# Kernel optimization log

Hardware: AMD Instinct MI355X
Metric: run time of the kernel (lower is better)

## Reference

```python
import jax, jax.numpy as jnp
import numpy as np

B, S, E, H = 8, 1024, 1024, 16
D = E // H          # head_dim = 64
FF = 4 * E          # mlp hidden = 4096
EPS = 1e-5


def setup_inputs() -> dict:
    key = jax.random.key(0)
    ks = jax.random.split(key, 12)
    s_e = 1.0 / np.sqrt(E)
    s_ff = 1.0 / np.sqrt(FF)
    return {
        "x": jax.random.normal(ks[0], (B, S, E), jnp.float32),
        # per-head q/k/v projections stacked: [H, E, D] (math layout: y = x @ W + b)
        "Wq": jax.random.normal(ks[1], (H, E, D), jnp.float32) * s_e,
        "bq": jnp.zeros((H, D), jnp.float32),
        "Wk": jax.random.normal(ks[2], (H, E, D), jnp.float32) * s_e,
        "bk": jnp.zeros((H, D), jnp.float32),
        "Wv": jax.random.normal(ks[3], (H, E, D), jnp.float32) * s_e,
        "bv": jnp.zeros((H, D), jnp.float32),
        # output projection [E, E]
        "Wo": jax.random.normal(ks[4], (E, E), jnp.float32) * s_e,
        "bo": jnp.zeros((E,), jnp.float32),
        # layernorms
        "g1": jnp.ones((E,), jnp.float32),
        "beta1": jnp.zeros((E,), jnp.float32),
        "g2": jnp.ones((E,), jnp.float32),
        "beta2": jnp.zeros((E,), jnp.float32),
        # MLP
        "W1": jax.random.normal(ks[5], (E, FF), jnp.float32) * s_e,
        "c1": jnp.zeros((FF,), jnp.float32),
        "W2": jax.random.normal(ks[6], (FF, E), jnp.float32) * s_ff,
        "c2": jnp.zeros((E,), jnp.float32),
    }


def _layernorm(x, g, b):
    mu = jnp.mean(x, axis=-1, keepdims=True)
    var = jnp.mean(jnp.square(x - mu), axis=-1, keepdims=True)
    return (x - mu) * jax.lax.rsqrt(var + EPS) * g + b


def _block(x, Wq, bq, Wk, bk, Wv, bv, Wo, bo, g1, beta1, g2, beta2, W1, c1, W2, c2):
    # --- attention sublayer (pre-norm) ---
    xn = _layernorm(x, g1, beta1)
    # all heads at once (equivalent to the per-head Python loop)
    q = jnp.einsum("bse,hed->bhsd", xn, Wq) + bq[:, None, :]
    k = jnp.einsum("bse,hed->bhsd", xn, Wk) + bk[:, None, :]
    v = jnp.einsum("bse,hed->bhsd", xn, Wv) + bv[:, None, :]
    scale = D ** -0.5
    scores = jnp.einsum("bhsd,bhtd->bhst", q, k) * scale  # [B,H,S,S]
    w = jax.nn.softmax(scores, axis=-1)
    ctx = jnp.einsum("bhst,bhtd->bhsd", w, v)             # [B,H,S,D]
    ctx = ctx.transpose(0, 2, 1, 3).reshape(x.shape[0], x.shape[1], E)  # concat heads
    attn_out = ctx @ Wo + bo
    x = x + attn_out
    # --- MLP sublayer (pre-norm) ---
    xn = _layernorm(x, g2, beta2)
    h = jax.nn.gelu(xn @ W1 + c1, approximate=False)
    return x + (h @ W2 + c2)


def reference(x, Wq, bq, Wk, bk, Wv, bv, Wo, bo, g1, beta1, g2, beta2, W1, c1, W2, c2):
    return _block(x, Wq, bq, Wk, bk, Wv, bv, Wo, bo, g1, beta1, g2, beta2, W1, c1, W2, c2)
```

## Files before the change

### kernel.cpp

```cpp
#include <hip/hip_runtime.h>
#include <math.h>


typedef _Float16 h16;
typedef __attribute__((ext_vector_type(8))) _Float16 f16x8;
typedef __attribute__((ext_vector_type(4))) float f32x4;

__device__ __forceinline__ void gl2lds16(const void* g, void* l) {
  __builtin_amdgcn_global_load_lds(
      (const __attribute__((address_space(1))) void*)g,
      (__attribute__((address_space(3))) void*)l, 16, 0, 0);
}

__global__ __launch_bounds__(256) void repack_kernel(
    const float* __restrict__ Wq, const float* __restrict__ Wk,
    const float* __restrict__ Wv, const float* __restrict__ Wo,
    const float* __restrict__ W1, const float* __restrict__ W2,
    const float* __restrict__ bq, const float* __restrict__ bk,
    const float* __restrict__ bv,
    h16* __restrict__ WqkvT, h16* __restrict__ WoT, h16* __restrict__ W1T,
    h16* __restrict__ W2T, float* __restrict__ bqkv)
{
  const int t = blockIdx.x;
  const int tid = threadIdx.x;
  if (t == 3072) {
    for (int i = tid; i < 3072; i += 256)
      bqkv[i] = (i < 1024) ? bq[i] : (i < 2048 ? bk[i - 1024] : bv[i - 2048]);
    return;
  }
  __shared__ float ld[64 * 65];

  const float* src; h16* dst;
  int sRS, dRS, k0, sn0, dn0;
  if (t < 768) {
    const int m = t >> 8, tt = t & 255, h = tt >> 4, tk = tt & 15;
    src = ((m == 0) ? Wq : (m == 1) ? Wk : Wv) + (size_t)h * 65536;
    dst = WqkvT; sRS = 64; dRS = 1024;
    k0 = tk * 64; sn0 = 0; dn0 = m * 1024 + h * 64;
  } else if (t < 1024) {
    const int tt = t - 768, tk = tt >> 4, tn = tt & 15;
    src = Wo; dst = WoT; sRS = 1024; dRS = 1024;
    k0 = tk * 64; sn0 = tn * 64; dn0 = tn * 64;
  } else if (t < 2048) {
    const int tt = t - 1024, tk = tt >> 6, tn = tt & 63;
    src = W1; dst = W1T; sRS = 4096; dRS = 1024;
    k0 = tk * 64; sn0 = tn * 64; dn0 = tn * 64;
  } else {
    const int tt = t - 2048, tk = tt >> 4, tn = tt & 15;
    src = W2; dst = W2T; sRS = 1024; dRS = 4096;
    k0 = tk * 64; sn0 = tn * 64; dn0 = tn * 64;
  }

  #pragma unroll
  for (int p = 0; p < 16; ++p) {
    const int idx = p * 256 + tid;
    const int r = idx >> 6, c = idx & 63;
    ld[c * 65 + r] = src[(size_t)(k0 + r) * sRS + sn0 + c];
  }
  __syncthreads();
  #pragma unroll
  for (int p = 0; p < 8; ++p) {
    const int idx = p * 512 + tid * 2;
    const int n = idx >> 6, k = idx & 63;
    union { unsigned int u; h16 e[2]; } pk;
    pk.e[0] = (h16)ld[n * 65 + k];
    pk.e[1] = (h16)ld[n * 65 + k + 1];
    *(unsigned int*)&dst[(size_t)(dn0 + n) * dRS + k0 + k] = pk.u;
  }
}

template <int IT>
__global__ __launch_bounds__(256) void ln_kernel(
    const void* __restrict__ in, const float* __restrict__ gw,
    const float* __restrict__ bw, h16* __restrict__ outp)
{
  const int row = blockIdx.x;
  const int tid = threadIdx.x;
  float v[4];
  if (IT == 0) {
    const float* p = (const float*)in + (size_t)row * 1024 + tid * 4;
    float4 tt = *(const float4*)p;
    v[0] = tt.x; v[1] = tt.y; v[2] = tt.z; v[3] = tt.w;
  } else {
    const h16* p = (const h16*)in + (size_t)row * 1024 + tid * 4;
    union { uint2 u; h16 h[4]; } raw;
    raw.u = *(const uint2*)p;
    v[0] = (float)raw.h[0]; v[1] = (float)raw.h[1];
    v[2] = (float)raw.h[2]; v[3] = (float)raw.h[3];
  }
  float s = v[0] + v[1] + v[2] + v[3];
  float ss = v[0]*v[0] + v[1]*v[1] + v[2]*v[2] + v[3]*v[3];
  #pragma unroll
  for (int off = 32; off >= 1; off >>= 1) {
    s += __shfl_down(s, off);
    ss += __shfl_down(ss, off);
  }
  __shared__ float red[8];
  const int w = tid >> 6;
  if ((tid & 63) == 0) { red[w] = s; red[4 + w] = ss; }
  __syncthreads();
  s = red[0] + red[1] + red[2] + red[3];
  ss = red[4] + red[5] + red[6] + red[7];
  const float mean = s * (1.0f / 1024.0f);
  const float var = ss * (1.0f / 1024.0f) - mean * mean;
  const float inv = rsqrtf(fmaxf(var, 0.0f) + 1e-5f);
  union { uint2 u; h16 h[4]; } pk;
  #pragma unroll
  for (int i = 0; i < 4; ++i)
    pk.h[i] = (h16)((v[i] - mean) * inv * gw[tid * 4 + i] + bw[tid * 4 + i]);
  *(uint2*)(outp + (size_t)row * 1024 + tid * 4) = pk.u;
}

template <int MODE>
__global__ __launch_bounds__(256) void gemm_bt(
    const h16* __restrict__ A, const h16* __restrict__ BT,
    const float* __restrict__ bias, const void* __restrict__ res,
    void* __restrict__ out, int M, int N, int K)
{
  __shared__ __align__(16) h16 As[128 * 32];
  __shared__ __align__(16) h16 Bs[128 * 32];
  const int tid = threadIdx.x;
  const int m0 = blockIdx.y * 128, n0 = blockIdx.x * 128;
  const int lane = tid & 63, w = tid >> 6;
  const int l15 = lane & 15, quad = lane >> 4;
  const int wm = (w >> 1) * 64, wn = (w & 1) * 64;

  f32x4 zero = {0.f, 0.f, 0.f, 0.f};
  f32x4 acc[4][4];
  #pragma unroll
  for (int a = 0; a < 4; ++a)
    #pragma unroll
    for (int b = 0; b < 4; ++b) acc[a][b] = zero;

  const int r0 = tid >> 2, kc0 = (tid & 3) * 8;
  const h16* Ag0 = A + (size_t)(m0 + r0) * K + kc0;
  const h16* Ag1 = A + (size_t)(m0 + r0 + 64) * K + kc0;
  const h16* Bg0 = BT + (size_t)(n0 + r0) * K + kc0;
  const h16* Bg1 = BT + (size_t)(n0 + r0 + 64) * K + kc0;
  h16* lA0 = As + w * 512;
  h16* lA1 = As + w * 512 + 2048;
  h16* lB0 = Bs + w * 512;
  h16* lB1 = Bs + w * 512 + 2048;

  for (int kt = 0; kt < K; kt += 32) {
    __syncthreads();
    gl2lds16(Ag0 + kt, lA0);
    gl2lds16(Ag1 + kt, lA1);
    gl2lds16(Bg0 + kt, lB0);
    gl2lds16(Bg1 + kt, lB1);
    __syncthreads();
    f16x8 af[4], bfr[4];
    #pragma unroll
    for (int i = 0; i < 4; ++i)
      af[i] = *(const f16x8*)&As[(wm + i * 16 + l15) * 32 + quad * 8];
    #pragma unroll
    for (int i = 0; i < 4; ++i)
      bfr[i] = *(const f16x8*)&Bs[(wn + i * 16 + l15) * 32 + quad * 8];
    #pragma unroll
    for (int mi = 0; mi < 4; ++mi)
      #pragma unroll
      for (int ni = 0; ni < 4; ++ni)
        acc[mi][ni] = __builtin_amdgcn_mfma_f32_16x16x32_f16(af[mi], bfr[ni], acc[mi][ni], 0, 0, 0);
  }

  #pragma unroll
  for (int mi = 0; mi < 4; ++mi) {
    #pragma unroll
    for (int ni = 0; ni < 4; ++ni) {
      #pragma unroll
      for (int i = 0; i < 4; ++i) {
        const int r = m0 + wm + mi * 16 + quad * 4 + i;
        const int c = n0 + wn + ni * 16 + l15;
        const size_t idx = (size_t)r * N + c;
        float v = acc[mi][ni][i] + bias[c];
        if (MODE == 0) {
          ((h16*)out)[idx] = (h16)v;
        } else if (MODE == 1) {
          v += ((const float*)res)[idx];
          ((h16*)out)[idx] = (h16)v;
        } else if (MODE == 2) {
          const float e = __expf(v * (-1.5957691216f - 0.0713548163f * v * v));
          v = v / (1.0f + e);
          ((h16*)out)[idx] = (h16)v;
        } else {
          v += (float)((const h16*)res)[idx];
          ((float*)out)[idx] = v;
        }
      }
    }
  }
}

__global__ __launch_bounds__(256, 2) void attn_kernel(
    const h16* __restrict__ qkv, h16* __restrict__ ctx)
{
  const int qb = blockIdx.x;
  const int bh = blockIdx.y;
  const int b = bh >> 4, h = bh & 15;
  const int tid = threadIdx.x;
  const int w = tid >> 6, lane = tid & 63;
  const int l15 = lane & 15, quad = lane >> 4;

  __shared__ __align__(16) h16 Ks[64 * 80];
  __shared__ __align__(16) h16 Vt[64 * 80];
  __shared__ __align__(16) h16 Ps[256 * 80];

  const size_t qrow0 = (size_t)(b * 1024 + qb * 256);
  for (int c = tid; c < 2048; c += 256) {
    const int row = c >> 3, kc = (c & 7) * 8;
    uint4 raw = *(const uint4*)(qkv + (qrow0 + row) * 3072 + h * 64 + kc);
    union { uint4 v; h16 e[8]; } in4, out4;
    in4.v = raw;
    #pragma unroll
    for (int i = 0; i < 8; ++i) out4.e[i] = in4.e[i] * (h16)0.125f;
    *(uint4*)&Ps[row * 80 + kc] = out4.v;
  }
  __syncthreads();
  f16x8 aq[4][2];
  #pragma unroll
  for (int r = 0; r < 4; ++r)
    #pragma unroll
    for (int s = 0; s < 2; ++s)
      aq[r][s] = *(const f16x8*)&Ps[(w * 64 + r * 16 + l15) * 80 + s * 32 + quad * 8];

  f32x4 zero = {0.f, 0.f, 0.f, 0.f};
  f32x4 o_acc[4][4];
  float l_p[4][4];
  #pragma unroll
  for (int r = 0; r < 4; ++r)
    #pragma unroll
    for (int i = 0; i < 4; ++i) { o_acc[r][i] = zero; l_p[r][i] = 0.f; }

  h16* Pw = &Ps[w * 64 * 80];

  for (int jt = 0; jt < 16; ++jt) {
    __syncthreads();
    const size_t kv0 = (size_t)(b * 1024 + jt * 64);
    for (int c = tid; c < 512; c += 256) {
      const int row = c >> 3, kc = (c & 7) * 8;
      *(uint4*)&Ks[row * 80 + kc] =
          *(const uint4*)(qkv + (kv0 + row) * 3072 + 1024 + h * 64 + kc);
    }
    #pragma unroll
    for (int cc = 0; cc < 2; ++cc) {
      const int d0 = (w + cc * 4) * 8;
      uint4 raw = *(const uint4*)(qkv + (kv0 + lane) * 3072 + 2048 + h * 64 + d0);
      union { uint4 v; h16 e[8]; } in4;
      in4.v = raw;
      #pragma unroll
      for (int i = 0; i < 8; ++i) Vt[(d0 + i) * 80 + lane] = in4.e[i];
    }
    __syncthreads();

    f16x8 kf[4][2];
    #pragma unroll
    for (int ni = 0; ni < 4; ++ni)
      #pragma unroll
      for (int s = 0; s < 2; ++s)
        kf[ni][s] = *(const f16x8*)&Ks[(ni * 16 + l15) * 80 + s * 32 + quad * 8];
    #pragma unroll
    for (int r = 0; r < 4; ++r) {
      f32x4 s_acc[4];
      #pragma unroll
      for (int i = 0; i < 4; ++i) s_acc[i] = zero;
      #pragma unroll
      for (int ni = 0; ni < 4; ++ni)
        #pragma unroll
        for (int s = 0; s < 2; ++s)
          s_acc[ni] = __builtin_amdgcn_mfma_f32_16x16x32_f16(aq[r][s], kf[ni][s], s_acc[ni], 0, 0, 0);
      #pragma unroll
      for (int ni = 0; ni < 4; ++ni)
        #pragma unroll
        for (int i = 0; i < 4; ++i) {
          float p = __expf(s_acc[ni][i]);
          l_p[r][i] += p;
          Pw[(r * 16 + quad * 4 + i) * 80 + ni * 16 + l15] = (h16)p;
        }
    }

    f16x8 vf[4][2];
    #pragma unroll
    for (int ni = 0; ni < 4; ++ni)
      #pragma unroll
      for (int s = 0; s < 2; ++s)
        vf[ni][s] = *(const f16x8*)&Vt[(ni * 16 + l15) * 80 + s * 32 + quad * 8];
    #pragma unroll
    for (int r = 0; r < 4; ++r) {
      f16x8 ap0 = *(const f16x8*)&Pw[(r * 16 + l15) * 80 + quad * 8];
      f16x8 ap1 = *(const f16x8*)&Pw[(r * 16 + l15) * 80 + 32 + quad * 8];
      #pragma unroll
      for (int ni = 0; ni < 4; ++ni) {
        o_acc[r][ni] = __builtin_amdgcn_mfma_f32_16x16x32_f16(ap0, vf[ni][0], o_acc[r][ni], 0, 0, 0);
        o_acc[r][ni] = __builtin_amdgcn_mfma_f32_16x16x32_f16(ap1, vf[ni][1], o_acc[r][ni], 0, 0, 0);
      }
    }
  }

  #pragma unroll
  for (int r = 0; r < 4; ++r)
    #pragma unroll
    for (int i = 0; i < 4; ++i) {
      float lt = l_p[r][i];
      #pragma unroll
      for (int off = 1; off < 16; off <<= 1) lt += __shfl_xor(lt, off);
      const float rinv = 1.0f / lt;
      const size_t row = qrow0 + w * 64 + r * 16 + quad * 4 + i;
      #pragma unroll
      for (int ni = 0; ni < 4; ++ni)
        ctx[row * 1024 + h * 64 + ni * 16 + l15] = (h16)(o_acc[r][ni][i] * rinv);
    }
}

extern "C" void kernel_launch(void* const* d_in, const int* in_sizes, int n_in,
                              void* d_out, int out_size, void* d_ws, size_t ws_size,
                              hipStream_t stream) {
  const float* x   = (const float*)d_in[0];
  const float* Wq  = (const float*)d_in[1];
  const float* bq  = (const float*)d_in[2];
  const float* Wk  = (const float*)d_in[3];
  const float* bk  = (const float*)d_in[4];
  const float* Wv  = (const float*)d_in[5];
  const float* bv  = (const float*)d_in[6];
  const float* Wo  = (const float*)d_in[7];
  const float* bo  = (const float*)d_in[8];
  const float* g1  = (const float*)d_in[9];
  const float* be1 = (const float*)d_in[10];
  const float* g2  = (const float*)d_in[11];
  const float* be2 = (const float*)d_in[12];
  const float* W1  = (const float*)d_in[13];
  const float* c1  = (const float*)d_in[14];
  const float* W2  = (const float*)d_in[15];
  const float* c2  = (const float*)d_in[16];

  char* ws = (char*)d_ws;
  h16*   WqkvT = (h16*)(ws + 0);
  h16*   WoT   = (h16*)(ws + 6291456);
  h16*   W1T   = (h16*)(ws + 8388608);
  h16*   W2T   = (h16*)(ws + 16777216);
  float* bqkv  = (float*)(ws + 25165824);
  h16*   bufA  = (h16*)(ws + 25178112);
  h16*   qkv   = (h16*)(ws + 41955328);
  h16*   x1    = (h16*)(ws + 41955328);
  h16*   hbuf  = (h16*)(ws + 58732544);

  repack_kernel<<<dim3(3073), dim3(256), 0, stream>>>(Wq, Wk, Wv, Wo, W1, W2, bq, bk, bv,
                                                      WqkvT, WoT, W1T, W2T, bqkv);
  ln_kernel<0><<<dim3(8192), dim3(256), 0, stream>>>(x, g1, be1, bufA);
  gemm_bt<0><<<dim3(24, 64), dim3(256), 0, stream>>>(bufA, WqkvT, bqkv, nullptr, qkv,
                                                     8192, 3072, 1024);
  attn_kernel<<<dim3(4, 128), dim3(256), 0, stream>>>(qkv, bufA);
  gemm_bt<1><<<dim3(8, 64), dim3(256), 0, stream>>>(bufA, WoT, bo, x, x1,
                                                    8192, 1024, 1024);
  ln_kernel<1><<<dim3(8192), dim3(256), 0, stream>>>(x1, g2, be2, bufA);
  gemm_bt<2><<<dim3(32, 64), dim3(256), 0, stream>>>(bufA, W1T, c1, nullptr, hbuf,
                                                     8192, 4096, 1024);
  gemm_bt<3><<<dim3(8, 64), dim3(256), 0, stream>>>(hbuf, W2T, c2, x1, d_out,
                                                    8192, 1024, 4096);
}
```

Baseline: 572.9 us.

## Rewrite GEMM with 256x128 tiles, triple-buffered LDS prefetch and swizzled layout

The fp16 MFMA GEMM moves from 256-thread 128x128 blocks with a K-step of 32 to 512-thread 256x128 blocks with a K-step of 64. Operands are loaded through a three-stage dynamic-LDS ring with a prefetch distance of two tiles, so global-to-LDS loads overlap MFMA work. The A and B prefetches are split around two compute halves, and s_setprio raises wave priority during the MFMA sections. An XOR swizzle on LDS columns is meant to avoid bank conflicts on fragment reads. The cost is about 144 KB of LDS per block, which allows only one block per CU, plus hand-placed waitcnt and barrier logic that is fragile.

New measurement: 511.6 us. 10.7% less time.

```diff
diff --git a/kernel.cpp b/kernel.cpp
--- a/kernel.cpp
+++ b/kernel.cpp
@@ -111,19 +111,33 @@
   *(uint2*)(outp + (size_t)row * 1024 + tid * 4) = pk.u;
 }
 
+#define GEMM_LDS 147456
+
 template <int MODE>
-__global__ __launch_bounds__(256) void gemm_bt(
+__global__ __launch_bounds__(512, 2) void gemm_bt(
     const h16* __restrict__ A, const h16* __restrict__ BT,
     const float* __restrict__ bias, const void* __restrict__ res,
     void* __restrict__ out, int M, int N, int K)
 {
-  __shared__ __align__(16) h16 As[128 * 32];
-  __shared__ __align__(16) h16 Bs[128 * 32];
+  extern __shared__ __align__(16) char smem[];
   const int tid = threadIdx.x;
-  const int m0 = blockIdx.y * 128, n0 = blockIdx.x * 128;
   const int lane = tid & 63, w = tid >> 6;
   const int l15 = lane & 15, quad = lane >> 4;
-  const int wm = (w >> 1) * 64, wn = (w & 1) * 64;
+  const int wm = w >> 1, wn = w & 1;
+  const int m0 = blockIdx.y * 256, n0 = blockIdx.x * 128;
+  const int NT = K >> 6;
+
+  const int srow = w * 8 + (lane >> 3);
+  const int scol = ((lane & 7) ^ ((lane >> 3) & 7)) * 8;
+  const h16* gA = A + (size_t)(m0 + srow) * K + scol;
+  const h16* gB = BT + (size_t)(n0 + srow) * K + scol;
+  const int ldsw = w * 1024;
+
+  const int arow = wm * 64 + l15;
+  const int brow = wn * 64 + l15;
+  const int x7 = l15 & 7;
+  const int sw0 = (quad ^ x7) << 4;
+  const int sw1 = ((4 | quad) ^ x7) << 4;
 
   f32x4 zero = {0.f, 0.f, 0.f, 0.f};
   f32x4 acc[4][4];
@@ -132,35 +146,86 @@
     #pragma unroll
     for (int b = 0; b < 4; ++b) acc[a][b] = zero;
 
-  const int r0 = tid >> 2, kc0 = (tid & 3) * 8;
-  const h16* Ag0 = A + (size_t)(m0 + r0) * K + kc0;
-  const h16* Ag1 = A + (size_t)(m0 + r0 + 64) * K + kc0;
-  const h16* Bg0 = BT + (size_t)(n0 + r0) * K + kc0;
-  const h16* Bg1 = BT + (size_t)(n0 + r0 + 64) * K + kc0;
-  h16* lA0 = As + w * 512;
-  h16* lA1 = As + w * 512 + 2048;
-  h16* lB0 = Bs + w * 512;
-  h16* lB1 = Bs + w * 512 + 2048;
-
-  for (int kt = 0; kt < K; kt += 32) {
-    __syncthreads();
-    gl2lds16(Ag0 + kt, lA0);
-    gl2lds16(Ag1 + kt, lA1);
-    gl2lds16(Bg0 + kt, lB0);
-    gl2lds16(Bg1 + kt, lB1);
-    __syncthreads();
-    f16x8 af[4], bfr[4];
-    #pragma unroll
-    for (int i = 0; i < 4; ++i)
-      af[i] = *(const f16x8*)&As[(wm + i * 16 + l15) * 32 + quad * 8];
-    #pragma unroll
-    for (int i = 0; i < 4; ++i)
-      bfr[i] = *(const f16x8*)&Bs[(wn + i * 16 + l15) * 32 + quad * 8];
+  {
+    char* b0 = smem;
+    char* b1 = smem + 49152;
+    #pragma unroll
+    for (int j = 0; j < 4; ++j) gl2lds16(gA + (size_t)j * 64 * K, b0 + j * 8192 + ldsw);
+    #pragma unroll
+    for (int j = 0; j < 2; ++j) gl2lds16(gB + (size_t)j * 64 * K, b0 + 32768 + j * 8192 + ldsw);
+    #pragma unroll
+    for (int j = 0; j < 4; ++j) gl2lds16(gA + 64 + (size_t)j * 64 * K, b1 + j * 8192 + ldsw);
+    #pragma unroll
+    for (int j = 0; j < 2; ++j) gl2lds16(gB + 64 + (size_t)j * 64 * K, b1 + 32768 + j * 8192 + ldsw);
+  }
+  asm volatile("s_waitcnt vmcnt(6)" ::: "memory");
+  __builtin_amdgcn_sched_barrier(0);
+  __builtin_amdgcn_s_barrier();
+
+  int cur = 0, pre = 2;
+  for (int t = 0; t < NT; ++t) {
+    const char* Ab = smem + cur * 49152;
+    const char* Bb = Ab + 32768;
+    char* Pb = smem + pre * 49152;
+    const bool pf = (t + 2) < NT;
+    f16x8 af[4][2], bf[4][2];
+
+    #pragma unroll
+    for (int mi = 0; mi < 4; ++mi) {
+      af[mi][0] = *(const f16x8*)(Ab + (arow + mi * 16) * 128 + sw0);
+      af[mi][1] = *(const f16x8*)(Ab + (arow + mi * 16) * 128 + sw1);
+    }
+    #pragma unroll
+    for (int ni = 0; ni < 2; ++ni) {
+      bf[ni][0] = *(const f16x8*)(Bb + (brow + ni * 16) * 128 + sw0);
+      bf[ni][1] = *(const f16x8*)(Bb + (brow + ni * 16) * 128 + sw1);
+    }
+    if (pf) {
+      const h16* g = gA + (size_t)(t + 2) * 64;
+      #pragma unroll
+      for (int j = 0; j < 4; ++j) gl2lds16(g + (size_t)j * 64 * K, Pb + j * 8192 + ldsw);
+    }
+    __builtin_amdgcn_s_barrier();
+    __builtin_amdgcn_s_setprio(1);
     #pragma unroll
     for (int mi = 0; mi < 4; ++mi)
       #pragma unroll
-      for (int ni = 0; ni < 4; ++ni)
-        acc[mi][ni] = __builtin_amdgcn_mfma_f32_16x16x32_f16(af[mi], bfr[ni], acc[mi][ni], 0, 0, 0);
+      for (int ni = 0; ni < 2; ++ni) {
+        acc[mi][ni] = __builtin_amdgcn_mfma_f32_16x16x32_f16(af[mi][0], bf[ni][0], acc[mi][ni], 0, 0, 0);
+        acc[mi][ni] = __builtin_amdgcn_mfma_f32_16x16x32_f16(af[mi][1], bf[ni][1], acc[mi][ni], 0, 0, 0);
+      }
+    __builtin_amdgcn_s_setprio(0);
+    __builtin_amdgcn_s_barrier();
+
+    #pragma unroll
+    for (int ni = 2; ni < 4; ++ni) {
+      bf[ni][0] = *(const f16x8*)(Bb + (brow + ni * 16) * 128 + sw0);
+      bf[ni][1] = *(const f16x8*)(Bb + (brow + ni * 16) * 128 + sw1);
+    }
+    if (pf) {
+      const h16* g = gB + (size_t)(t + 2) * 64;
+      #pragma unroll
+      for (int j = 0; j < 2; ++j) gl2lds16(g + (size_t)j * 64 * K, Pb + 32768 + j * 8192 + ldsw);
+    }
+    __builtin_amdgcn_s_barrier();
+    __builtin_amdgcn_s_setprio(1);
+    #pragma unroll
+    for (int mi = 0; mi < 4; ++mi)
+      #pragma unroll
+      for (int ni = 2; ni < 4; ++ni) {
+        acc[mi][ni] = __builtin_amdgcn_mfma_f32_16x16x32_f16(af[mi][0], bf[ni][0], acc[mi][ni], 0, 0, 0);
+        acc[mi][ni] = __builtin_amdgcn_mfma_f32_16x16x32_f16(af[mi][1], bf[ni][1], acc[mi][ni], 0, 0, 0);
+      }
+    __builtin_amdgcn_s_setprio(0);
+    if (pf) {
+      asm volatile("s_waitcnt vmcnt(6)" ::: "memory");
+    } else if (t + 2 == NT) {
+      asm volatile("s_waitcnt vmcnt(0)" ::: "memory");
+    }
+    __builtin_amdgcn_sched_barrier(0);
+    __builtin_amdgcn_s_barrier();
+    cur = (cur == 2) ? 0 : cur + 1;
+    pre = (pre == 2) ? 0 : pre + 1;
   }
 
   #pragma unroll
@@ -169,8 +234,8 @@
     for (int ni = 0; ni < 4; ++ni) {
       #pragma unroll
       for (int i = 0; i < 4; ++i) {
-        const int r = m0 + wm + mi * 16 + quad * 4 + i;
-        const int c = n0 + wn + ni * 16 + l15;
+        const int r = m0 + wm * 64 + mi * 16 + quad * 4 + i;
+        const int c = n0 + wn * 64 + ni * 16 + l15;
         const size_t idx = (size_t)r * N + c;
         float v = acc[mi][ni][i] + bias[c];
         if (MODE == 0) {
@@ -343,17 +408,26 @@
   h16*   x1    = (h16*)(ws + 41955328);
   h16*   hbuf  = (h16*)(ws + 58732544);
 
+  static bool attr_done = false;
+  if (!attr_done) {
+    hipFuncSetAttribute((const void*)gemm_bt<0>, hipFuncAttributeMaxDynamicSharedMemorySize, GEMM_LDS);
+    hipFuncSetAttribute((const void*)gemm_bt<1>, hipFuncAttributeMaxDynamicSharedMemorySize, GEMM_LDS);
+    hipFuncSetAttribute((const void*)gemm_bt<2>, hipFuncAttributeMaxDynamicSharedMemorySize, GEMM_LDS);
+    hipFuncSetAttribute((const void*)gemm_bt<3>, hipFuncAttributeMaxDynamicSharedMemorySize, GEMM_LDS);
+    attr_done = true;
+  }
+
   repack_kernel<<<dim3(3073), dim3(256), 0, stream>>>(Wq, Wk, Wv, Wo, W1, W2, bq, bk, bv,
                                                       WqkvT, WoT, W1T, W2T, bqkv);
   ln_kernel<0><<<dim3(8192), dim3(256), 0, stream>>>(x, g1, be1, bufA);
-  gemm_bt<0><<<dim3(24, 64), dim3(256), 0, stream>>>(bufA, WqkvT, bqkv, nullptr, qkv,
-                                                     8192, 3072, 1024);
+  gemm_bt<0><<<dim3(24, 32), dim3(512), GEMM_LDS, stream>>>(bufA, WqkvT, bqkv, nullptr, qkv,
+                                                            8192, 3072, 1024);
   attn_kernel<<<dim3(4, 128), dim3(256), 0, stream>>>(qkv, bufA);
-  gemm_bt<1><<<dim3(8, 64), dim3(256), 0, stream>>>(bufA, WoT, bo, x, x1,
-                                                    8192, 1024, 1024);
+  gemm_bt<1><<<dim3(8, 32), dim3(512), GEMM_LDS, stream>>>(bufA, WoT, bo, x, x1,
+                                                           8192, 1024, 1024);
   ln_kernel<1><<<dim3(8192), dim3(256), 0, stream>>>(x1, g2, be2, bufA);
-  gemm_bt<2><<<dim3(32, 64), dim3(256), 0, stream>>>(bufA, W1T, c1, nullptr, hbuf,
-                                                     8192, 4096, 1024);
-  gemm_bt<3><<<dim3(8, 64), dim3(256), 0, stream>>>(hbuf, W2T, c2, x1, d_out,
-                                                    8192, 1024, 4096);
-}
+  gemm_bt<2><<<dim3(32, 32), dim3(512), GEMM_LDS, stream>>>(bufA, W1T, c1, nullptr, hbuf,
+                                                            8192, 4096, 1024);
+  gemm_bt<3><<<dim3(8, 32), dim3(512), GEMM_LDS, stream>>>(hbuf, W2T, c2, x1, d_out,
+                                                           8192, 1024, 4096);
+}
```
